# Optimization experiments

Measured on AMD Instinct MI355X. Metric: run time of the kernel, lower is better.

The kernel has to match this reference:

```python
import jax, jax.numpy as jnp
import numpy as np
from jax import lax

CORR = 5        # patch_size of correlation (5x5 displacements)
PAD = (CORR - 1) // 2
SEQ_IDS = [0, 1, 3, 4]  # gating_seq_len=5, center frame index 2 is skipped


def conv2d(x, w, b):
    # 3x3, stride 1, padding 1 == SAME; NCHW / OIHW
    y = lax.conv_general_dilated(x, w, (1, 1), 'SAME',
                                 dimension_numbers=('NCHW', 'OIHW', 'NCHW'))
    return y + b[None, :, None, None]


def _xavier(k, shape):
    fan_in = shape[1] * shape[2] * shape[3]
    fan_out = shape[0] * shape[2] * shape[3]
    limit = float(np.sqrt(6.0 / (fan_in + fan_out)))
    return jax.random.uniform(k, shape, jnp.float32, -limit, limit)


def setup_inputs() -> dict:
    key = jax.random.key(0)
    ks = jax.random.split(key, 4)
    B, C, H, W = 2, 512, 64, 64
    x = jax.random.normal(ks[0], (5, B, C, H, W), jnp.float32)
    Wg = jnp.stack([_xavier(k, (2, 2 * C, 3, 3)) for k in jax.random.split(ks[1], 4)])
    bg = jnp.zeros((4, 2), jnp.float32)
    Wd = jnp.stack([_xavier(k, (C, 2 * C, 3, 3)) for k in jax.random.split(ks[2], 4)])
    bd = jnp.zeros((4, C), jnp.float32)
    Wc = _xavier(ks[3], (C, 4 * C, 3, 3))
    bc = jnp.zeros((C,), jnp.float32)
    return dict(x=x, Wg=Wg, bg=bg, Wd=Wd, bd=bd, Wc=Wc, bc=bc)


def _align(feat2, feat1):
    # spatial_correlation_sample(feat2, feat1, kernel=1, patch=5, pad=0):
    # corr[b, d, y, x] = sum_c feat2[b,c,y,x] * feat1[b,c,y+di,x+dj], di,dj in [-2,2]
    b, c, h, w = feat1.shape
    pad1 = jnp.pad(feat1, ((0, 0), (0, 0), (PAD, PAD), (PAD, PAD)))
    corr = jnp.stack([jnp.sum(feat2 * pad1[:, :, i:i + h, j:j + w], axis=1)
                      for i in range(CORR) for j in range(CORR)], axis=1)  # [b,25,h,w]
    # torch F.softmax default dim for 4D is dim=1; scaled by 20/global-max
    attn = jax.nn.softmax(corr * (20.0 / jnp.max(corr)), axis=1)
    # shifted-window weighted sum over the 25 displacements
    new_feat = jnp.zeros_like(feat1)
    for i in range(CORR):
        for j in range(CORR):
            new_feat = new_feat + attn[:, i * CORR + j][:, None] * pad1[:, :, i:i + h, j:j + w]
    return new_feat


def reference(x, Wg, bg, Wd, bd, Wc, bc):
    center = x[2]                       # feat2 = middle frame for every pair
    C = center.shape[1]
    gated = []
    for n, s in enumerate(SEQ_IDS):
        new_feat = _align(center, x[s])
        feat = jnp.concatenate([center, new_feat], axis=1)          # [B,2C,H,W]
        gw = jax.nn.sigmoid(conv2d(feat, Wg[n], bg[n]))              # [B,2,H,W]
        fg = jnp.concatenate([center * gw[:, 0:1], new_feat * gw[:, 1:2]], axis=1)
        gated.append(jax.nn.relu(conv2d(fg, Wd[n], bd[n])))          # [B,C,H,W]
    total = jnp.concatenate(gated, axis=1)                           # [B,4C,H,W]
    return jax.nn.relu(conv2d(total, Wc, bc))
```

## Files before the change

kernel.cpp:

```cpp
#include <hip/hip_runtime.h>
#include <hip/hip_bf16.h>
#include <stdint.h>

typedef __attribute__((ext_vector_type(8))) short bf16x8;
typedef __attribute__((ext_vector_type(4))) float f32x4;
typedef __attribute__((ext_vector_type(4))) int int4v;

#define DEVI static __device__ __forceinline__

DEVI unsigned short f2b(float f) {
  union { float f; unsigned u; } v; v.f = f;
  unsigned r = (v.u + 0x7FFFu + ((v.u >> 16) & 1u)) >> 16;
  return (unsigned short)r;
}
DEVI float b2f(unsigned short h) {
  union { unsigned u; float f; } v; v.u = ((unsigned)h) << 16;
  return v.f;
}
DEVI unsigned encf(float f) {
  union { float f; unsigned u; } v; v.f = f;
  return (v.u & 0x80000000u) ? ~v.u : (v.u | 0x80000000u);
}
DEVI float decf(unsigned u) {
  union { unsigned u; float f; } v;
  v.u = (u & 0x80000000u) ? (u & 0x7FFFFFFFu) : ~u;
  return v.f;
}
DEVI void gload16(const void* g, void* l) {
  __builtin_amdgcn_global_load_lds(
      (const __attribute__((address_space(1))) unsigned int*)g,
      (__attribute__((address_space(3))) unsigned int*)l, 16, 0, 0);
}

__global__ __launch_bounds__(256) void k_reorder_w2(const float* __restrict__ src,
                                                    unsigned short* __restrict__ dst,
                                                    int CI) {
  int r = blockIdx.x;
  int t = threadIdx.x;
  const float* s = src + (size_t)r * CI * 9;
  unsigned short* d = dst + (size_t)r * CI * 9;
  for (int ci0 = 0; ci0 < CI; ci0 += 256) {
    int ci = ci0 + t;
    float v[9];
#pragma unroll
    for (int k = 0; k < 9; k++) v[k] = s[(size_t)ci * 9 + k];
    unsigned short* db = d + (size_t)(ci >> 5) * 288 + (ci & 31);
#pragma unroll
    for (int k = 0; k < 9; k++) db[(size_t)k * 32] = f2b(v[k]);
  }
}

__global__ void k_reorder_wg(const float* __restrict__ src, float* __restrict__ dst) {
  int idx = blockIdx.x * 256 + threadIdx.x;
  int ci = idx & 1023;
  int rt = idx >> 10;
  int tap = rt % 9;
  int po = rt / 9;
  dst[(((size_t)po * 9 + tap) * 32 + (ci & 31)) * 32 + (ci >> 5)] =
      src[((size_t)po * 1024 + ci) * 9 + tap];
}

__global__ void k_border(unsigned short* __restrict__ p, int H, int wpad, int C8,
                         int nImg) {
  int inner = H - 2 * wpad;
  int borderPx = H * H - inner * inner;
  long total = (long)borderPx * C8 * nImg;
  int topN = wpad * H;
  for (long i = (long)blockIdx.x * 256 + threadIdx.x; i < total;
       i += (long)gridDim.x * 256) {
    int c = (int)(i % C8);
    long r2 = i / C8;
    int px = (int)(r2 % borderPx);
    int img = (int)(r2 / borderPx);
    int y, x;
    if (px < topN) {
      y = px / H; x = px % H;
    } else if (px < 2 * topN) {
      int q = px - topN; y = H - 1 - (q / H); x = q % H;
    } else {
      int q = px - 2 * topN;
      int row = q / (2 * wpad), cc = q % (2 * wpad);
      y = wpad + row;
      x = cc < wpad ? cc : H - 2 * wpad + cc;
    }
    *(int4v*)&p[((((size_t)img * H + y) * H + x) * C8 + c) * 8] = int4v{0, 0, 0, 0};
  }
}

__global__ __launch_bounds__(256) void k_pad(const float* __restrict__ xin,
                                             unsigned short* __restrict__ xf1,
                                             unsigned short* __restrict__ cp) {
  __shared__ unsigned short lds[64 * 66];
  int t = threadIdx.x;
  int y = blockIdx.x;
  int fb = blockIdx.y;
  int f = fb >> 1, b = fb & 1;
  const float* src = xin + (size_t)fb * 512 * 4096 + y * 64;
  unsigned short* base;
  if (f == 2) {
    base = cp + (((size_t)b * 66) + y + 1) * 66 * 512 + 512;
  } else {
    int fi = f < 2 ? f : f - 1;
    base = xf1 + (((size_t)(fi * 2 + b) * 68) + y + 2) * 68 * 512 + 2 * 512;
  }
  for (int c0 = 0; c0 < 512; c0 += 64) {
#pragma unroll
    for (int r = 0; r < 16; ++r) {
      int ci = r * 4 + (t >> 6);
      int xx = t & 63;
      lds[ci * 66 + xx] = f2b(src[(size_t)(c0 + ci) * 4096 + xx]);
    }
    __syncthreads();
    int xp = t >> 2;
    int cc = (t & 3) * 16;
    __align__(16) unsigned short vals[16];
#pragma unroll
    for (int i = 0; i < 16; i++) vals[i] = lds[(cc + i) * 66 + xp];
    unsigned short* dst = base + (size_t)xp * 512 + c0 + cc;
    *(int4v*)(dst) = *(const int4v*)(vals);
    *(int4v*)(dst + 8) = *(const int4v*)(vals + 8);
    __syncthreads();
  }
}

__global__ __launch_bounds__(256) void k_corr(const float* __restrict__ xin,
                                              float* __restrict__ corrpart) {
  __shared__ float f1h[840];
  int t = threadIdx.x;
  int tx = t & 15, ty = t >> 4;
  int x0 = blockIdx.x * 16, y0 = blockIdx.y * 16;
  int z = blockIdx.z;
  int b = z & 1, pair = (z >> 1) & 3, part = z >> 3;
  int s = pair < 2 ? pair : pair + 1;
  const float* f2 = xin + ((size_t)(2 * 2 + b) * 512) * 4096;
  const float* f1 = xin + ((size_t)(s * 2 + b) * 512) * 4096;

  int cnt = (t < 32) ? 4 : 3;
  int ldso[4], goff[4], chv[4];
  bool val[4];
#pragma unroll
  for (int q = 0; q < 4; q++) {
    int k = t + q * 256;
    if (k >= 800) k = 799;
    int ch = k >= 400;
    int e = k - ch * 400;
    int r = e / 20, cc = e - r * 20;
    int gy = y0 + r - 2, gx = x0 + cc - 2;
    val[q] = ((unsigned)gy < 64u) && ((unsigned)gx < 64u);
    ldso[q] = ch * 420 + r * 21 + cc;
    goff[q] = gy * 64 + gx;
    chv[q] = ch;
  }

  float acc[25];
#pragma unroll
  for (int d = 0; d < 25; d++) acc[d] = 0.f;
  int y = y0 + ty, x = x0 + tx;
  for (int c = part * 128; c < part * 128 + 128; c += 2) {
#pragma unroll
    for (int q = 0; q < 4; q++) {
      if (q < cnt) {
        float v = 0.f;
        if (val[q]) v = f1[(size_t)(c + chv[q]) * 4096 + goff[q]];
        f1h[ldso[q]] = v;
      }
    }
    float f2a = f2[(size_t)c * 4096 + y * 64 + x];
    float f2c = f2[(size_t)(c + 1) * 4096 + y * 64 + x];
    __syncthreads();
#pragma unroll
    for (int d = 0; d < 25; ++d) {
      int di = d / 5, dj = d % 5;
      acc[d] += f2a * f1h[(ty + di) * 21 + tx + dj] +
                f2c * f1h[420 + (ty + di) * 21 + tx + dj];
    }
    __syncthreads();
  }
  float* out = corrpart + ((size_t)((part * 4 + pair) * 2 + b) * 25) * 4096;
#pragma unroll
  for (int d = 0; d < 25; d++) out[(size_t)d * 4096 + y * 64 + x] = acc[d];
}

__global__ __launch_bounds__(256) void k_corr_combine(const float* __restrict__ cpart,
                                                      float* __restrict__ corr,
                                                      unsigned* __restrict__ maxb) {
  const size_t PERPAIR = (size_t)2 * 25 * 4096;
  int pair = blockIdx.y;
  size_t i4 = ((size_t)blockIdx.x * 256 + threadIdx.x) * 4;
  f32x4 sacc = {0.f, 0.f, 0.f, 0.f};
#pragma unroll
  for (int p = 0; p < 4; p++)
    sacc += *(const f32x4*)(cpart + ((size_t)(p * 4 + pair)) * PERPAIR + i4);
  *(f32x4*)(corr + (size_t)pair * PERPAIR + i4) = sacc;
  float m = fmaxf(fmaxf(sacc[0], sacc[1]), fmaxf(sacc[2], sacc[3]));
#pragma unroll
  for (int off = 32; off; off >>= 1) m = fmaxf(m, __shfl_xor(m, off));
  __shared__ float wm[4];
  if ((threadIdx.x & 63) == 0) wm[threadIdx.x >> 6] = m;
  __syncthreads();
  if (threadIdx.x == 0) {
    float mm = fmaxf(fmaxf(wm[0], wm[1]), fmaxf(wm[2], wm[3]));
    atomicMax(maxb + pair, encf(mm));
  }
}

__global__ __launch_bounds__(256) void k_attn3(const unsigned short* __restrict__ xf1,
                                               const float* __restrict__ corr,
                                               const unsigned* __restrict__ maxb,
                                               unsigned short* __restrict__ nfpad) {
  __shared__ unsigned short f1t[400 * 8];
  int t = threadIdx.x;
  int tx = t & 15, ty = t >> 4;
  int x0 = blockIdx.x * 16, y0 = blockIdx.y * 16;
  int z = blockIdx.z;
  int b = z & 1, pair = (z >> 1) & 3, cgh = z >> 3;
  const unsigned short* f1 = xf1 + ((size_t)(pair * 2 + b)) * 68 * 68 * 512;
  int y = y0 + ty, x = x0 + tx;
  const float* cr = corr + ((size_t)(pair * 2 + b)) * 25 * 4096 + y * 64 + x;

  int r0 = t / 20, c0 = t - r0 * 20;
  size_t go0 = ((size_t)(y0 + r0) * 68 + (x0 + c0)) * 512;
  bool has1 = t < 144;
  int k1 = t + 256;
  int r1 = k1 / 20, c1 = k1 - r1 * 20;
  size_t go1 = ((size_t)(y0 + r1) * 68 + (x0 + c1)) * 512;

  float p[25];
  float mx = -1e30f;
#pragma unroll
  for (int d = 0; d < 25; d++) {
    p[d] = cr[(size_t)d * 4096];
    mx = fmaxf(mx, p[d]);
  }
  float gs = 20.f / decf(maxb[pair]);
  float ss = 0.f;
#pragma unroll
  for (int d = 0; d < 25; d++) {
    p[d] = __expf((p[d] - mx) * gs);
    ss += p[d];
  }
  float inv = 1.f / ss;
#pragma unroll
  for (int d = 0; d < 25; d++) p[d] *= inv;

  for (int q = 0; q < 4; ++q) {
    int cg = cgh * 4 + q;
    *(int4v*)&f1t[t * 8] = *(const int4v*)&f1[go0 + cg * 8];
    if (has1) *(int4v*)&f1t[k1 * 8] = *(const int4v*)&f1[go1 + cg * 8];
    __syncthreads();
    float acc[8] = {0.f, 0.f, 0.f, 0.f, 0.f, 0.f, 0.f, 0.f};
#pragma unroll
    for (int d = 0; d < 25; d++) {
      bf16x8 v = *(const bf16x8*)&f1t[((ty + d / 5) * 20 + tx + d % 5) * 8];
      float pd = p[d];
#pragma unroll
      for (int e = 0; e < 8; e++) acc[e] += pd * b2f((unsigned short)v[e]);
    }
    __align__(16) unsigned short o[8];
#pragma unroll
    for (int e = 0; e < 8; e++) o[e] = f2b(acc[e]);
    *(int4v*)&nfpad[(((size_t)(pair * 2 + b) * 66 + (y + 1)) * 66 + (x + 1)) * 512 +
                    cg * 8] = *(const int4v*)o;
    __syncthreads();
  }
}

__global__ __launch_bounds__(256) void k_gate3(const unsigned short* __restrict__ cp,
                                               const unsigned short* __restrict__ nfp,
                                               const float* __restrict__ wgt,
                                               const float* __restrict__ bg,
                                               float* __restrict__ gw) {
  int t = threadIdx.x;
  int z = blockIdx.z;
  int b = z & 1, pair = z >> 1;
  int y = blockIdx.y;
  int x = blockIdx.x * 8 + (t >> 5);
  int chunk = t & 31;
  int ci0 = chunk * 32;
  int half = ci0 >> 9;
  int ch0 = ci0 & 511;
  const unsigned short* src = half ? (nfp + ((size_t)(pair * 2 + b)) * 66 * 66 * 512)
                                   : (cp + ((size_t)b) * 66 * 66 * 512);
  const float* w0b = wgt + ((size_t)(pair * 2 + 0) * 9) * 1024;
  const float* w1b = wgt + ((size_t)(pair * 2 + 1) * 9) * 1024;
  float a0 = 0.f, a1 = 0.f;
  for (int tap = 0; tap < 9; ++tap) {
    int ky = tap / 3, kx = tap % 3;
    const unsigned short* ip = src + ((size_t)(y + ky) * 66 + (x + kx)) * 512 + ch0;
    const float* w0 = w0b + tap * 1024 + chunk;
    const float* w1 = w1b + tap * 1024 + chunk;
#pragma unroll
    for (int q = 0; q < 4; ++q) {
      bf16x8 v8 = *(const bf16x8*)(ip + q * 8);
#pragma unroll
      for (int e = 0; e < 8; e++) {
        float f = b2f((unsigned short)v8[e]);
        a0 += f * w0[(q * 8 + e) * 32];
        a1 += f * w1[(q * 8 + e) * 32];
      }
    }
  }
#pragma unroll
  for (int md = 1; md < 32; md <<= 1) {
    a0 += __shfl_xor(a0, md);
    a1 += __shfl_xor(a1, md);
  }
  if ((t & 31) == 0) {
    float g0 = 1.f / (1.f + __expf(-(a0 + bg[pair * 2 + 0])));
    float g1 = 1.f / (1.f + __expf(-(a1 + bg[pair * 2 + 1])));
    gw[(((size_t)(pair * 2 + b) * 2 + 0) * 64 + y) * 64 + x] = g0;
    gw[(((size_t)(pair * 2 + b) * 2 + 1) * 64 + y) * 64 + x] = g1;
  }
}

__global__ __launch_bounds__(256) void k_fg(const unsigned short* __restrict__ cp,
                                            const unsigned short* __restrict__ nfp,
                                            const float* __restrict__ gw,
                                            unsigned short* __restrict__ fgp, int pairBase) {
  int pz = blockIdx.y;
  int pair = pairBase + pz;
  unsigned short* dstBase = fgp + (size_t)pz * 2 * 66 * 66 * 1024;
  size_t idx = (size_t)blockIdx.x * 256 + threadIdx.x;
  int chunk = (int)(idx & 127);
  size_t px = idx >> 7;
  int b = (int)(px >> 12), rem = (int)(px & 4095);
  int y = rem >> 6, x = rem & 63;
  int ci0 = chunk * 8;
  int half = ci0 >> 9;
  float g = gw[(((size_t)(pair * 2 + b) * 2 + half) * 64 + y) * 64 + x];
  const unsigned short* src = half ? (nfp + ((size_t)(pair * 2 + b)) * 66 * 66 * 512)
                                   : (cp + (size_t)b * 66 * 66 * 512);
  size_t poff = ((size_t)(y + 1) * 66 + (x + 1)) * 512 + (ci0 - half * 512);
  bf16x8 v = *(const bf16x8*)(src + poff);
  __align__(16) unsigned short o[8];
#pragma unroll
  for (int e = 0; e < 8; e++) o[e] = f2b(b2f((unsigned short)v[e]) * g);
  *(int4v*)(dstBase + ((size_t)(b * 66 + y + 1) * 66 + (x + 1)) * 1024 + ci0) =
      *(const int4v*)o;
}

template <int CI, int MODE>
__global__ __launch_bounds__(512) void conv5(const unsigned short* __restrict__ inB,
                                             const unsigned short* __restrict__ WTb,
                                             const float* __restrict__ bias,
                                             unsigned short* __restrict__ outB,
                                             unsigned short* __restrict__ outP,
                                             int pairOfs, int multiz) {
  constexpr int K = 9 * CI;
  constexpr int KTOT = K / 64;
  constexpr int KT = (MODE == 2) ? KTOT / 4 : KTOT;
  __shared__ unsigned short As[2 * 2 * 8192];
  __shared__ unsigned short Bs[2 * 2 * 8192];

  int t = threadIdx.x;
  int bid = blockIdx.x;
  int xcd = bid & 7;
  int z, m, n;
  if (multiz) {
    z = xcd >> 1; m = xcd & 1; n = bid >> 3;
  } else {
    z = 0; m = bid & 1; n = bid >> 1;
  }
  const unsigned short* inPad = (MODE == 0) ? inB + (size_t)z * 2 * 66 * 66 * 1024 : inB;
  const unsigned short* WT = (MODE == 0) ? WTb + (size_t)z * 512 * 9216 : WTb;
  const int kt0 = (MODE == 2) ? z * KT : 0;
  const int ktEnd = kt0 + KT;
  int co0 = m * 256, n0 = n * 256;

  int rowS[2], kcS[2], linS[2];
  size_t bpix2[2][2];
#pragma unroll
  for (int rr = 0; rr < 2; rr++) {
    int idx2 = rr * 512 + t;
    rowS[rr] = idx2 >> 3;
    kcS[rr] = (idx2 & 7) ^ (rowS[rr] & 7);
    linS[rr] = idx2 * 8;
#pragma unroll
    for (int h = 0; h < 2; h++) {
      int ng = n0 + h * 128 + rowS[rr];
      int bb = ng >> 12, yy = (ng >> 6) & 63, xx = ng & 63;
      bpix2[h][rr] = (size_t)((bb * 66 + yy) * 66 + xx) * CI + (kcS[rr] & 3) * 8;
    }
  }

  f32x4 acc[8][4];
#pragma unroll
  for (int i = 0; i < 8; i++)
#pragma unroll
    for (int j = 0; j < 4; j++) acc[i][j] = f32x4{0.f, 0.f, 0.f, 0.f};

  int wid = t >> 6, l = t & 63;
  int wm = wid >> 2, wn = wid & 3;
  int lrow = l & 15, lk4 = l >> 4;

  auto stA = [&](int bufp, int h, int kt) {
#pragma unroll
    for (int rr = 0; rr < 2; rr++)
      gload16(WT + (size_t)(co0 + h * 128 + rowS[rr]) * K + kt * 64 + kcS[rr] * 8,
              &As[(bufp * 2 + h) * 8192 + linS[rr]]);
  };
  auto stB = [&](int bufp, int h, int kt) {
    int g0 = kt * 2, g1 = g0 + 1;
    int cib0 = g0 / 9, tap0 = g0 - cib0 * 9;
    int cib1 = g1 / 9, tap1 = g1 - cib1 * 9;
    int off0 = ((tap0 / 3) * 66 + tap0 % 3) * CI + cib0 * 32;
    int off1 = ((tap1 / 3) * 66 + tap1 % 3) * CI + cib1 * 32;
#pragma unroll
    for (int rr = 0; rr < 2; rr++)
      gload16(inPad + bpix2[h][rr] + ((kcS[rr] & 4) ? off1 : off0),
              &Bs[(bufp * 2 + h) * 8192 + linS[rr]]);
  };

  bf16x8 afr0[4][2], afr1[4][2], bfr0[2][2], bfr1[2][2];

#define RDA(DST, C, MH)                                                         \
  _Pragma("unroll") for (int ii = 0; ii < 4; ++ii) {                            \
    int row = (MH)*64 + ii * 16 + lrow;                                         \
    _Pragma("unroll") for (int kk = 0; kk < 2; ++kk) {                          \
      int pos = (kk * 4 + lk4) ^ (lrow & 7);                                    \
      DST[ii][kk] = *(const bf16x8*)&As[((C)*2 + wm) * 8192 + row * 64 + pos * 8]; \
    }                                                                           \
  }
#define RDB(DST, C, NH)                                                         \
  _Pragma("unroll") for (int j = 0; j < 2; ++j) {                               \
    int row = (wn & 1) * 64 + (NH)*32 + j * 16 + lrow;                          \
    _Pragma("unroll") for (int kk = 0; kk < 2; ++kk) {                          \
      int pos = (kk * 4 + lk4) ^ (lrow & 7);                                    \
      DST[j][kk] =                                                              \
          *(const bf16x8*)&Bs[((C)*2 + (wn >> 1)) * 8192 + row * 64 + pos * 8]; \
    }                                                                           \
  }
#define QUAD(AF, BF, MH, NH)                                                    \
  __builtin_amdgcn_s_setprio(1);                                                \
  _Pragma("unroll") for (int ii = 0; ii < 4; ++ii) {                            \
    _Pragma("unroll") for (int j = 0; j < 2; ++j) {                             \
      _Pragma("unroll") for (int kk = 0; kk < 2; ++kk) {                        \
        acc[(MH)*4 + ii][(NH)*2 + j] = __builtin_amdgcn_mfma_f32_16x16x32_bf16( \
            AF[ii][kk], BF[j][kk], acc[(MH)*4 + ii][(NH)*2 + j], 0, 0, 0);      \
      }                                                                         \
    }                                                                           \
  }                                                                             \
  __builtin_amdgcn_s_setprio(0);
#define DRAIN_LGKM asm volatile("s_waitcnt lgkmcnt(0)" ::: "memory");

  {
    int b0 = kt0 & 1, b1 = b0 ^ 1;
    stA(b0, 0, kt0); stA(b0, 1, kt0); stB(b0, 0, kt0); stB(b0, 1, kt0);
    stA(b1, 0, kt0 + 1); stA(b1, 1, kt0 + 1); stB(b1, 0, kt0 + 1); stB(b1, 1, kt0 + 1);
    asm volatile("s_waitcnt vmcnt(8)" ::: "memory");
    __builtin_amdgcn_s_barrier();
  }

  for (int kt = kt0; kt < ktEnd; ++kt) {
    int cur = kt & 1;
    const bool pf = (kt + 2 < ktEnd);
    RDA(afr0, cur, 0);
    RDB(bfr0, cur, 0);
    QUAD(afr0, bfr0, 0, 0)
    RDA(afr1, cur, 1);
    QUAD(afr1, bfr0, 1, 0)
    DRAIN_LGKM
    __builtin_amdgcn_s_barrier();
    if (pf) { stA(cur, 0, kt + 2); stA(cur, 1, kt + 2); }
    RDB(bfr1, cur, 1);
    QUAD(afr1, bfr1, 1, 1)
    DRAIN_LGKM
    __builtin_amdgcn_s_barrier();
    if (pf) { stB(cur, 0, kt + 2); stB(cur, 1, kt + 2); }
    QUAD(afr0, bfr1, 0, 1)
    if (pf) {
      asm volatile("s_waitcnt vmcnt(8)" ::: "memory");
    } else {
      asm volatile("s_waitcnt vmcnt(0)" ::: "memory");
    }
    __builtin_amdgcn_s_barrier();
  }
#undef RDA
#undef RDB
#undef QUAD
#undef DRAIN_LGKM

#pragma unroll
  for (int i = 0; i < 8; i++) {
#pragma unroll
    for (int j = 0; j < 4; j++) {
      int col = wn * 64 + j * 16 + lrow;
      int ng = n0 + col;
      int bb = ng >> 12, yy = (ng >> 6) & 63, xx = ng & 63;
#pragma unroll
      for (int r = 0; r < 4; r++) {
        int row = wm * 128 + i * 16 + lk4 * 4 + r;
        int co = co0 + row;
        if (MODE == 0) {
          int zc = (z + pairOfs) * 512 + co;
          float v = acc[i][j][r] + bias[zc];
          v = v > 0.f ? v : 0.f;
          outB[((size_t)(bb * 66 + yy + 1) * 66 + (xx + 1)) * 2048 + zc] = f2b(v);
        } else {
          outP[((size_t)(z * 512 + co) << 13) + ng] = f2b(acc[i][j][r]);
        }
      }
    }
  }
}

__global__ __launch_bounds__(256) void k_combine2(const unsigned short* __restrict__ p,
                                                  const float* __restrict__ bc,
                                                  float* __restrict__ out) {
  size_t i8 = ((size_t)blockIdx.x * 256 + threadIdx.x) * 8;
  int co = (int)(i8 >> 13);
  int ng = (int)(i8 & 8191);
  float s[8] = {0.f, 0.f, 0.f, 0.f, 0.f, 0.f, 0.f, 0.f};
#pragma unroll
  for (int zz = 0; zz < 4; zz++) {
    bf16x8 v = *(const bf16x8*)&p[((size_t)(zz * 512 + co) << 13) + ng];
#pragma unroll
    for (int e = 0; e < 8; e++) s[e] += b2f((unsigned short)v[e]);
  }
  float bb = bc[co];
  int batch = ng >> 12, rem = ng & 4095;
  float* o = out + (((size_t)(batch * 512 + co)) << 12) + rem;
#pragma unroll
  for (int e = 0; e < 8; e++) {
    float q = s[e] + bb;
    o[e] = q > 0.f ? q : 0.f;
  }
}

extern "C" void kernel_launch(void* const* d_in, const int* in_sizes, int n_in,
                              void* d_out, int out_size, void* d_ws, size_t ws_size,
                              hipStream_t stream) {
  const float* x = (const float*)d_in[0];
  const float* Wg = (const float*)d_in[1];
  const float* bg = (const float*)d_in[2];
  const float* Wd = (const float*)d_in[3];
  const float* bd = (const float*)d_in[4];
  const float* Wc = (const float*)d_in[5];
  const float* bc = (const float*)d_in[6];
  float* out = (float*)d_out;

  char* ws = (char*)d_ws;
  size_t off = 0;
  auto alloc = [&](size_t bytes) {
    void* p = ws + off;
    off = (off + bytes + 255) & ~(size_t)255;
    return p;
  };
  const size_t SZ_WDT = (size_t)2048 * 9216 * 2;
  const size_t SZ_WCT = (size_t)512 * 18432 * 2;
  const size_t SZ_WGT = (size_t)4 * 2 * 9 * 1024 * 4;
  const size_t SZ_CP = (size_t)2 * 66 * 66 * 512 * 2;
  const size_t SZ_NF = (size_t)4 * 2 * 66 * 66 * 512 * 2;
  const size_t SZ_GT = (size_t)2 * 66 * 66 * 2048 * 2;
  const size_t SZ_GW = (size_t)4 * 2 * 2 * 4096 * 4;
  const size_t SZ_XF1 = (size_t)4 * 2 * 68 * 68 * 512 * 2;
  const size_t SZ_CORR = (size_t)4 * 2 * 25 * 4096 * 4;
  const size_t SZ_FG1 = (size_t)2 * 66 * 66 * 1024 * 2;
  const size_t SZ_FG4 = SZ_FG1 * 4;

  unsigned short* WdT = (unsigned short*)alloc(SZ_WDT);
  unsigned short* WcT = (unsigned short*)alloc(SZ_WCT);
  float* WgT = (float*)alloc(SZ_WGT);
  unsigned short* centerpad = (unsigned short*)alloc(SZ_CP);
  unsigned short* nfpad = (unsigned short*)alloc(SZ_NF);
  unsigned short* gatedpad = (unsigned short*)alloc(SZ_GT);
  float* gw = (float*)alloc(SZ_GW);
  unsigned* maxb = (unsigned*)alloc(256);

  size_t unionOff = off;
  unsigned short* xf1 = (unsigned short*)(ws + unionOff);
  size_t o2 = unionOff + ((SZ_XF1 + 255) & ~(size_t)255);
  float* corr = (float*)(ws + o2);
  float* cpart = (float*)(ws + o2 + ((SZ_CORR + 255) & ~(size_t)255));
  unsigned short* fg = (unsigned short*)(ws + unionOff);
  unsigned short* wcp = (unsigned short*)(ws + unionOff);
  bool batched = ws_size >= unionOff + SZ_FG4;

  hipMemsetAsync(maxb, 0, 64, stream);

  k_border<<<512, 256, 0, stream>>>(xf1, 68, 2, 64, 8);
  k_border<<<512, 256, 0, stream>>>(centerpad, 66, 1, 64, 2);
  k_border<<<512, 256, 0, stream>>>(nfpad, 66, 1, 64, 8);
  k_border<<<512, 256, 0, stream>>>(gatedpad, 66, 1, 256, 2);

  k_reorder_w2<<<2048, 256, 0, stream>>>(Wd, WdT, 1024);
  k_reorder_w2<<<512, 256, 0, stream>>>(Wc, WcT, 2048);
  k_reorder_wg<<<288, 256, 0, stream>>>(Wg, WgT);
  k_pad<<<dim3(64, 10), 256, 0, stream>>>(x, xf1, centerpad);
  k_corr<<<dim3(4, 4, 32), 256, 0, stream>>>(x, cpart);
  k_corr_combine<<<dim3(200, 4), 256, 0, stream>>>(cpart, corr, maxb);
  k_attn3<<<dim3(4, 4, 128), 256, 0, stream>>>(xf1, corr, maxb, nfpad);
  k_gate3<<<dim3(8, 64, 8), 256, 0, stream>>>(centerpad, nfpad, WgT, bg, gw);

  k_border<<<512, 256, 0, stream>>>(fg, 66, 1, 128, batched ? 8 : 2);

  if (batched) {
    k_fg<<<dim3(4096, 4), 256, 0, stream>>>(centerpad, nfpad, gw, fg, 0);
    conv5<1024, 0><<<256, 512, 0, stream>>>(fg, WdT, bd, gatedpad, nullptr, 0, 1);
  } else {
    for (int pair = 0; pair < 4; ++pair) {
      k_fg<<<dim3(4096, 1), 256, 0, stream>>>(centerpad, nfpad, gw, fg, pair);
      conv5<1024, 0><<<64, 512, 0, stream>>>(
          fg, WdT + (size_t)pair * 512 * 9216, bd, gatedpad, nullptr, pair, 0);
    }
  }
  conv5<2048, 2><<<256, 512, 0, stream>>>(gatedpad, WcT, nullptr, nullptr, wcp, 0, 1);
  k_combine2<<<2048, 256, 0, stream>>>(wcp, bc, out);
}
```

Baseline: 786.5 us.

## Split final conv K eight ways, trim GEMM barriers, interleave corr LDS channels

In the batched path, the final 2048-channel conv now uses 512 blocks with an 8-way K split instead of 4-way, and the combine kernel sums 8 partials. This gives more parallel work across the GPU, at the cost of a larger bf16 partial buffer and more combine traffic. The conv5 main loop reads both B fragments before the first barrier and issues all A/B prefetch stores after it, removing one barrier and one LDS drain per k-step. The correlation kernel stores the two channels as interleaved float2 in shared memory, so each displacement needs one LDS read instead of two. The larger partial buffer also assumes the workspace was sized for 8 partials.

```diff
diff --git a/kernel.cpp b/kernel.cpp
--- a/kernel.cpp
+++ b/kernel.cpp
@@ -4,6 +4,7 @@
 
 typedef __attribute__((ext_vector_type(8))) short bf16x8;
 typedef __attribute__((ext_vector_type(4))) float f32x4;
+typedef __attribute__((ext_vector_type(2))) float f32x2;
 typedef __attribute__((ext_vector_type(4))) int int4v;
 
 #define DEVI static __device__ __forceinline__
@@ -125,7 +126,7 @@
 
 __global__ __launch_bounds__(256) void k_corr(const float* __restrict__ xin,
                                               float* __restrict__ corrpart) {
-  __shared__ float f1h[840];
+  __shared__ f32x2 f1h2[420];
   int t = threadIdx.x;
   int tx = t & 15, ty = t >> 4;
   int x0 = blockIdx.x * 16, y0 = blockIdx.y * 16;
@@ -135,34 +136,38 @@
   const float* f2 = xin + ((size_t)(2 * 2 + b) * 512) * 4096;
   const float* f1 = xin + ((size_t)(s * 2 + b) * 512) * 4096;
 
-  int cnt = (t < 32) ? 4 : 3;
-  int ldso[4], goff[4], chv[4];
-  bool val[4];
-#pragma unroll
-  for (int q = 0; q < 4; q++) {
-    int k = t + q * 256;
-    if (k >= 800) k = 799;
-    int ch = k >= 400;
-    int e = k - ch * 400;
-    int r = e / 20, cc = e - r * 20;
-    int gy = y0 + r - 2, gx = x0 + cc - 2;
-    val[q] = ((unsigned)gy < 64u) && ((unsigned)gx < 64u);
-    ldso[q] = ch * 420 + r * 21 + cc;
-    goff[q] = gy * 64 + gx;
-    chv[q] = ch;
-  }
+  int r0 = t / 20, c0 = t - r0 * 20;
+  int ls0 = r0 * 21 + c0;
+  int gy0 = y0 + r0 - 2, gx0 = x0 + c0 - 2;
+  bool val0 = ((unsigned)gy0 < 64u) && ((unsigned)gx0 < 64u);
+  int go0 = gy0 * 64 + gx0;
+  bool has1 = t < 144;
+  int s1 = t + 256;
+  int r1 = s1 / 20, c1 = s1 - r1 * 20;
+  int ls1 = r1 * 21 + c1;
+  int gy1 = y0 + r1 - 2, gx1 = x0 + c1 - 2;
+  bool val1 = ((unsigned)gy1 < 64u) && ((unsigned)gx1 < 64u);
+  int go1 = gy1 * 64 + gx1;
 
   float acc[25];
 #pragma unroll
   for (int d = 0; d < 25; d++) acc[d] = 0.f;
   int y = y0 + ty, x = x0 + tx;
   for (int c = part * 128; c < part * 128 + 128; c += 2) {
-#pragma unroll
-    for (int q = 0; q < 4; q++) {
-      if (q < cnt) {
-        float v = 0.f;
-        if (val[q]) v = f1[(size_t)(c + chv[q]) * 4096 + goff[q]];
-        f1h[ldso[q]] = v;
+    {
+      float a0 = 0.f, b0v = 0.f;
+      if (val0) {
+        a0 = f1[(size_t)c * 4096 + go0];
+        b0v = f1[(size_t)(c + 1) * 4096 + go0];
+      }
+      f1h2[ls0] = f32x2{a0, b0v};
+      if (has1) {
+        float a1 = 0.f, b1v = 0.f;
+        if (val1) {
+          a1 = f1[(size_t)c * 4096 + go1];
+          b1v = f1[(size_t)(c + 1) * 4096 + go1];
+        }
+        f1h2[ls1] = f32x2{a1, b1v};
       }
     }
     float f2a = f2[(size_t)c * 4096 + y * 64 + x];
@@ -171,8 +176,8 @@
 #pragma unroll
     for (int d = 0; d < 25; ++d) {
       int di = d / 5, dj = d % 5;
-      acc[d] += f2a * f1h[(ty + di) * 21 + tx + dj] +
-                f2c * f1h[420 + (ty + di) * 21 + tx + dj];
+      f32x2 v = f1h2[(ty + di) * 21 + tx + dj];
+      acc[d] += f2a * v[0] + f2c * v[1];
     }
     __syncthreads();
   }
@@ -345,22 +350,24 @@
                                              const float* __restrict__ bias,
                                              unsigned short* __restrict__ outB,
                                              unsigned short* __restrict__ outP,
-                                             int pairOfs, int multiz) {
+                                             int pairOfs, int multiz, int nz) {
   constexpr int K = 9 * CI;
   constexpr int KTOT = K / 64;
-  constexpr int KT = (MODE == 2) ? KTOT / 4 : KTOT;
   __shared__ unsigned short As[2 * 2 * 8192];
   __shared__ unsigned short Bs[2 * 2 * 8192];
 
   int t = threadIdx.x;
   int bid = blockIdx.x;
-  int xcd = bid & 7;
   int z, m, n;
-  if (multiz) {
+  if (multiz == 2) {
+    z = bid & 7; m = (bid >> 3) & 1; n = bid >> 4;
+  } else if (multiz == 1) {
+    int xcd = bid & 7;
     z = xcd >> 1; m = xcd & 1; n = bid >> 3;
   } else {
     z = 0; m = bid & 1; n = bid >> 1;
   }
+  const int KT = (MODE == 2) ? KTOT / nz : KTOT;
   const unsigned short* inPad = (MODE == 0) ? inB + (size_t)z * 2 * 66 * 66 * 1024 : inB;
   const unsigned short* WT = (MODE == 0) ? WTb + (size_t)z * 512 * 9216 : WTb;
   const int kt0 = (MODE == 2) ? z * KT : 0;
@@ -456,17 +463,17 @@
     const bool pf = (kt + 2 < ktEnd);
     RDA(afr0, cur, 0);
     RDB(bfr0, cur, 0);
+    RDB(bfr1, cur, 1);
     QUAD(afr0, bfr0, 0, 0)
     RDA(afr1, cur, 1);
     QUAD(afr1, bfr0, 1, 0)
     DRAIN_LGKM
     __builtin_amdgcn_s_barrier();
-    if (pf) { stA(cur, 0, kt + 2); stA(cur, 1, kt + 2); }
-    RDB(bfr1, cur, 1);
+    if (pf) {
+      stA(cur, 0, kt + 2); stA(cur, 1, kt + 2);
+      stB(cur, 0, kt + 2); stB(cur, 1, kt + 2);
+    }
     QUAD(afr1, bfr1, 1, 1)
-    DRAIN_LGKM
-    __builtin_amdgcn_s_barrier();
-    if (pf) { stB(cur, 0, kt + 2); stB(cur, 1, kt + 2); }
     QUAD(afr0, bfr1, 0, 1)
     if (pf) {
       asm volatile("s_waitcnt vmcnt(8)" ::: "memory");
@@ -506,13 +513,12 @@
 
 __global__ __launch_bounds__(256) void k_combine2(const unsigned short* __restrict__ p,
                                                   const float* __restrict__ bc,
-                                                  float* __restrict__ out) {
+                                                  float* __restrict__ out, int nz) {
   size_t i8 = ((size_t)blockIdx.x * 256 + threadIdx.x) * 8;
   int co = (int)(i8 >> 13);
   int ng = (int)(i8 & 8191);
   float s[8] = {0.f, 0.f, 0.f, 0.f, 0.f, 0.f, 0.f, 0.f};
-#pragma unroll
-  for (int zz = 0; zz < 4; zz++) {
+  for (int zz = 0; zz < nz; zz++) {
     bf16x8 v = *(const bf16x8*)&p[((size_t)(zz * 512 + co) << 13) + ng];
 #pragma unroll
     for (int e = 0; e < 8; e++) s[e] += b2f((unsigned short)v[e]);
@@ -596,14 +602,16 @@
 
   if (batched) {
     k_fg<<<dim3(4096, 4), 256, 0, stream>>>(centerpad, nfpad, gw, fg, 0);
-    conv5<1024, 0><<<256, 512, 0, stream>>>(fg, WdT, bd, gatedpad, nullptr, 0, 1);
+    conv5<1024, 0><<<256, 512, 0, stream>>>(fg, WdT, bd, gatedpad, nullptr, 0, 1, 1);
+    conv5<2048, 2><<<512, 512, 0, stream>>>(gatedpad, WcT, nullptr, nullptr, wcp, 0, 2, 8);
+    k_combine2<<<2048, 256, 0, stream>>>(wcp, bc, out, 8);
   } else {
     for (int pair = 0; pair < 4; ++pair) {
       k_fg<<<dim3(4096, 1), 256, 0, stream>>>(centerpad, nfpad, gw, fg, pair);
       conv5<1024, 0><<<64, 512, 0, stream>>>(
-          fg, WdT + (size_t)pair * 512 * 9216, bd, gatedpad, nullptr, pair, 0);
-    }
-  }
-  conv5<2048, 2><<<256, 512, 0, stream>>>(gatedpad, WcT, nullptr, nullptr, wcp, 0, 1);
-  k_combine2<<<2048, 256, 0, stream>>>(wcp, bc, out);
-}
+          fg, WdT + (size_t)pair * 512 * 9216, bd, gatedpad, nullptr, pair, 0, 1);
+    }
+    conv5<2048, 2><<<256, 512, 0, stream>>>(gatedpad, WcT, nullptr, nullptr, wcp, 0, 1, 4);
+    k_combine2<<<2048, 256, 0, stream>>>(wcp, bc, out, 4);
+  }
+}
```

Result: no change. 772.4 us (-1.8%).
